# Performance work log

Hardware: AMD Instinct MI355X
Metric: run time of the kernel (lower is better)

## Reference

```python
import jax, jax.numpy as jnp
import numpy as np

N, D, DPE, H = 4096, 256, 16, 8
HD = D // H
SCALE = HD ** -0.5


def setup_inputs() -> dict:
    key = jax.random.key(0)
    ks = jax.random.split(key, 10)
    s = lambda fan_in: 1.0 / np.sqrt(fan_in)
    return {
        "x": jax.random.normal(ks[0], (N, D), jnp.float32),
        "pe": jax.random.normal(ks[1], (N, DPE), jnp.float32),
        "Wqkv": jax.random.uniform(ks[2], (D, 3 * D), jnp.float32, -s(D), s(D)),
        "bqkv": jax.random.uniform(ks[3], (3 * D,), jnp.float32, -s(D), s(D)),
        "Wpe": jax.random.uniform(ks[4], (DPE, H), jnp.float32, -s(DPE), s(DPE)),
        "bpe": jax.random.uniform(ks[5], (H,), jnp.float32, -s(DPE), s(DPE)),
        "Wout": jax.random.uniform(ks[6], (D, D), jnp.float32, -s(D), s(D)),
        "bout": jax.random.uniform(ks[7], (D,), jnp.float32, -s(D), s(D)),
    }


def reference(x, pe, Wqkv, bqkv, Wpe, bpe, Wout, bout):
    # qkv: [N, 3, H, HD] -> q,k,v each [H, N, HD]
    qkv = (x @ Wqkv + bqkv).reshape(N, 3, H, HD).transpose(1, 2, 0, 3)
    q, k, v = qkv[0], qkv[1], qkv[2]
    # attention scores [H, N, N]
    attn = jnp.einsum("hnd,hmd->hnm", q, k) * SCALE
    # pairwise PE-difference bias: bias[h,i,j] = pe_proj[i,h] - pe_proj[j,h]
    pe_proj = pe @ Wpe + bpe  # [N, H]
    pe_bias = (pe_proj[:, None, :] - pe_proj[None, :, :]).transpose(2, 0, 1)
    attn = jax.nn.softmax(attn + pe_bias, axis=-1)
    # dropout disabled (eval mode, p=0)
    out = jnp.einsum("hnm,hmd->nhd", attn, v).reshape(N, D)
    return out @ Wout + bout
```

## Files before the change

kernel.cpp:

```cpp
#include <hip/hip_runtime.h>
#include <math.h>

#define NN 4096
#define HH 8
constexpr float SCALE = 0.17677669529663687f;
constexpr float LOG2E = 1.4426950408889634f;
constexpr float SC2   = SCALE * LOG2E;

typedef __bf16 bf16;
typedef __bf16 bf16x8 __attribute__((ext_vector_type(8)));
typedef __bf16 bf16x4 __attribute__((ext_vector_type(4)));
typedef float  f32x4  __attribute__((ext_vector_type(4)));

#define MFMA(a, b, c) __builtin_amdgcn_mfma_f32_16x16x32_bf16((a), (b), (c), 0, 0, 0)

template <int K, int N, bool SCALEQ>
__device__ __forceinline__ void wcast_body(const float* __restrict__ W,
                                           bf16* __restrict__ WhT,
                                           bf16* __restrict__ WlT,
                                           int n0, int k0, int t,
                                           float (*tile)[65]) {
#pragma unroll
    for (int p = 0; p < 16; ++p) {
        const int r = p * 4 + (t >> 6);
        const int c = t & 63;
        tile[r][c] = W[(size_t)(k0 + r) * N + n0 + c];
    }
    __syncthreads();
    const int nr = t >> 2, kc0 = (t & 3) * 16;
    const float sc = (SCALEQ && (n0 + nr) < 256) ? SC2 : 1.0f;
    bf16x8 h[2], l[2];
#pragma unroll
    for (int g = 0; g < 2; ++g)
#pragma unroll
        for (int j = 0; j < 8; ++j) {
            const float v = tile[kc0 + g * 8 + j][nr] * sc;
            const bf16 hh = (bf16)v;
            h[g][j] = hh;
            l[g][j] = (bf16)(v - (float)hh);
        }
    const size_t ob = (size_t)(n0 + nr) * K + k0 + kc0;
    *(bf16x8*)&WhT[ob] = h[0];
    *(bf16x8*)&WhT[ob + 8] = h[1];
    *(bf16x8*)&WlT[ob] = l[0];
    *(bf16x8*)&WlT[ob + 8] = l[1];
}

__global__ __launch_bounds__(256) void preproc_kernel(
    const float* __restrict__ x, const float* __restrict__ Wqkv,
    const float* __restrict__ Wout, const float* __restrict__ bqkv,
    const float* __restrict__ pe, const float* __restrict__ Wpe,
    const float* __restrict__ bpe,
    bf16* __restrict__ xh, bf16* __restrict__ xl,
    bf16* __restrict__ WqkvhT, bf16* __restrict__ WqkvlT,
    bf16* __restrict__ WouthT, bf16* __restrict__ WoutlT,
    float* __restrict__ bqkv_s, float* __restrict__ ep) {
    __shared__ float tile[64][65];
    const int b = blockIdx.x, t = threadIdx.x;
    if (b < 1024) {
        const int i = (b * 256 + t) * 4;
        const float4 v = *(const float4*)&x[i];
        bf16x4 h, l;
        const float vv[4] = {v.x, v.y, v.z, v.w};
#pragma unroll
        for (int r = 0; r < 4; ++r) {
            h[r] = (bf16)vv[r];
            l[r] = (bf16)(vv[r] - (float)h[r]);
        }
        *(bf16x4*)&xh[i] = h;
        *(bf16x4*)&xl[i] = l;
    } else if (b < 1072) {
        const int bb = b - 1024;
        wcast_body<256, 768, true>(Wqkv, WqkvhT, WqkvlT, (bb % 12) * 64, (bb / 12) * 64, t, tile);
    } else if (b < 1088) {
        const int bb = b - 1072;
        wcast_body<256, 256, false>(Wout, WouthT, WoutlT, (bb % 4) * 64, (bb / 4) * 64, t, tile);
    } else if (b < 1216) {
        const int idx = (b - 1088) * 256 + t;
        const int h = idx >> 12;
        const int n = idx & 4095;
        float acc = bpe[h];
#pragma unroll
        for (int k = 0; k < 16; ++k) acc += pe[n * 16 + k] * Wpe[k * 8 + h];
        ep[h * NN + n] = __builtin_amdgcn_exp2f(-acc * LOG2E - 8.0f);
    } else {
        for (int i = t; i < 768; i += 256)
            bqkv_s[i] = bqkv[i] * (i < 256 ? SC2 : 1.0f);
    }
}

template <int NOUT, int NTILE, typename OT>
__global__ __launch_bounds__(256, 2) void gemm3s_kernel(const bf16* __restrict__ Ah,
                                                        const bf16* __restrict__ Al,
                                                        const bf16* __restrict__ BhT,
                                                        const bf16* __restrict__ BlT,
                                                        const float* __restrict__ bias,
                                                        OT* __restrict__ C) {
    constexpr int NS = NTILE / 16;
    const int t = threadIdx.x, wave = t >> 6, lane = t & 63;
    const int quad = lane >> 4, i16 = lane & 15;
    const int m0 = blockIdx.x * 128 + wave * 32;
    const int n0 = blockIdx.y * NTILE;

    __shared__ __align__(16) bf16 Bs[NTILE * 512];

    {
        const int l = t & 63, i16l = l & 15, ql = l >> 4;
#pragma unroll
        for (int c = t >> 6; c < NS * 16; c += 4) {
            const bool lo = c >= NS * 8;
            const int cc = lo ? c - NS * 8 : c;
            const int nsi = cc >> 3, kc = cc & 7;
            const bf16* src = (lo ? BlT : BhT) +
                (size_t)(n0 + nsi * 16 + i16l) * 256 + kc * 32 + ql * 8;
            *(uint4*)&Bs[c * 512 + l * 8] = *(const uint4*)src;
        }
    }

    bf16x8 ah[2][8], al[2][8];
#pragma unroll
    for (int ms = 0; ms < 2; ++ms) {
        const size_t abase = (size_t)(m0 + ms * 16 + i16) * 256 + quad * 8;
#pragma unroll
        for (int kc = 0; kc < 8; ++kc) {
            ah[ms][kc] = *(const bf16x8*)&Ah[abase + kc * 32];
            al[ms][kc] = *(const bf16x8*)&Al[abase + kc * 32];
        }
    }
    __syncthreads();

#pragma unroll
    for (int nsi = 0; nsi < NS; ++nsi) {
        f32x4 acc[2];
        acc[0] = f32x4{0.f, 0.f, 0.f, 0.f};
        acc[1] = f32x4{0.f, 0.f, 0.f, 0.f};
#pragma unroll
        for (int kc = 0; kc < 8; ++kc) {
            const bf16x8 bh = *(const bf16x8*)&Bs[(nsi * 8 + kc) * 512 + lane * 8];
            const bf16x8 bl = *(const bf16x8*)&Bs[((NS + nsi) * 8 + kc) * 512 + lane * 8];
            acc[0] = MFMA(ah[0][kc], bh, acc[0]);
            acc[0] = MFMA(ah[0][kc], bl, acc[0]);
            acc[0] = MFMA(al[0][kc], bh, acc[0]);
            acc[1] = MFMA(ah[1][kc], bh, acc[1]);
            acc[1] = MFMA(ah[1][kc], bl, acc[1]);
            acc[1] = MFMA(al[1][kc], bh, acc[1]);
        }
        const int n = n0 + nsi * 16 + i16;
        const float b = bias[n];
#pragma unroll
        for (int ms = 0; ms < 2; ++ms)
#pragma unroll
            for (int r = 0; r < 4; ++r)
                C[(size_t)(m0 + ms * 16 + quad * 4 + r) * NOUT + n] = (OT)(acc[ms][r] + b);
    }
}

__global__ __launch_bounds__(256) void kvtrans_kernel(const bf16* __restrict__ qkvb,
                                                      const float* __restrict__ ep,
                                                      bf16* __restrict__ Kf,
                                                      bf16* __restrict__ Vf) {
    const int t = threadIdx.x;
    const int kt = blockIdx.y, h = blockIdx.x;
    __shared__ __align__(16) bf16 Ktile[64 * 32];
    __shared__ __align__(16) bf16 Vtile[64 * 32];
    __shared__ float eps[64];
    {
        const int tok = kt * 64 + (t >> 2);
        const int d8 = (t & 3) * 8;
        *(uint4*)&Ktile[(t >> 2) * 32 + d8] =
            *(const uint4*)&qkvb[(size_t)tok * 768 + 256 + h * 32 + d8];
        *(uint4*)&Vtile[(t >> 2) * 32 + d8] =
            *(const uint4*)&qkvb[(size_t)tok * 768 + 512 + h * 32 + d8];
        if (t < 64) eps[t] = ep[h * NN + kt * 64 + t];
    }
    __syncthreads();
    {
        const int s = t >> 6, l = t & 63, quad = l >> 4, i16 = l & 15;
        bf16x8 o;
#pragma unroll
        for (int j = 0; j < 8; ++j) o[j] = Ktile[(s * 16 + i16) * 32 + quad * 8 + j];
        *(bf16x8*)&Kf[((size_t)(h * 64 + kt) * 4 + s) * 512 + l * 8] = o;
    }
    for (int c = t; c < 384; c += 256) {
        const int ch = c >> 6, ll = c & 63, qd = ll >> 4, ii = ll & 15;
        const int dt = ch >> 1, kc = ch & 1;
        const int dimp = dt * 16 + ii;
        bf16x8 o;
#pragma unroll
        for (int j = 0; j < 8; ++j) {
            const int key = kc * 32 + qd * 8 + j;
            float v;
            if (dimp < 32)       v = (float)Vtile[key * 32 + dimp] * eps[key];
            else if (dimp == 32) v = eps[key];
            else                 v = 0.f;
            o[j] = (bf16)v;
        }
        *(bf16x8*)&Vf[((size_t)(h * 64 + kt) * 6 + ch) * 512 + ll * 8] = o;
    }
}

__global__ __launch_bounds__(256, 2) void attn_kernel(const bf16* __restrict__ qkvb,
                                                      const bf16* __restrict__ Kf,
                                                      const bf16* __restrict__ Vf,
                                                      bf16* __restrict__ aoh,
                                                      bf16* __restrict__ aol) {
    const int t = threadIdx.x, kh = t >> 6, lane = t & 63;
    const int quad = lane >> 4, i16 = lane & 15;
    const int qb = blockIdx.y, h = blockIdx.x;

    __shared__ __align__(16) bf16 Pt[4][4][16 * 72];
    __shared__ __align__(16) float Mrg[3][64][48];

    const int q0 = qb * 64;
    bf16x8 qf[4];
#pragma unroll
    for (int qs = 0; qs < 4; ++qs)
        qf[qs] = *(const bf16x8*)&qkvb[(size_t)(q0 + qs * 16 + i16) * 768 + h * 32 + quad * 8];

    f32x4 o[3][4];
#pragma unroll
    for (int dt = 0; dt < 3; ++dt)
#pragma unroll
        for (int qs = 0; qs < 4; ++qs) o[dt][qs] = f32x4{0.f, 0.f, 0.f, 0.f};

    const bf16* kb = Kf + (size_t)(h * 64) * 2048 + lane * 8;
    const bf16* vb = Vf + (size_t)(h * 64) * 3072 + lane * 8;

    const int kt0 = kh * 16;
    bf16x8 kcur[4];
#pragma unroll
    for (int s = 0; s < 4; ++s)
        kcur[s] = *(const bf16x8*)&kb[((size_t)kt0 * 4 + s) * 512];

    for (int it = 0; it < 16; ++it) {
        const int kt = kt0 + it;
        bf16x8 vv[6];
#pragma unroll
        for (int c = 0; c < 6; ++c)
            vv[c] = *(const bf16x8*)&vb[((size_t)kt * 6 + c) * 512];
        bf16x8 knx[4];
        if (it < 15) {
#pragma unroll
            for (int s = 0; s < 4; ++s)
                knx[s] = *(const bf16x8*)&kb[((size_t)(kt + 1) * 4 + s) * 512];
        } else {
#pragma unroll
            for (int s = 0; s < 4; ++s) knx[s] = kcur[s];
        }

        const f32x4 z = {0.f, 0.f, 0.f, 0.f};
#pragma unroll
        for (int qh = 0; qh < 2; ++qh) {
            f32x4 sf[2][4];
#pragma unroll
            for (int ks = 0; ks < 4; ++ks) {
                sf[0][ks] = MFMA(kcur[ks], qf[qh * 2 + 0], z);
                sf[1][ks] = MFMA(kcur[ks], qf[qh * 2 + 1], z);
            }
#pragma unroll
            for (int qi = 0; qi < 2; ++qi) {
                const int qs = qh * 2 + qi;
#pragma unroll
                for (int ks = 0; ks < 4; ++ks) {
                    bf16x4 pk;
#pragma unroll
                    for (int r = 0; r < 4; ++r)
                        pk[r] = (bf16)__builtin_amdgcn_exp2f(sf[qi][ks][r]);
                    *(bf16x4*)&Pt[kh][qs][i16 * 72 + ks * 16 + quad * 4] = pk;
                }
            }
        }
        asm volatile("s_waitcnt lgkmcnt(0)" ::: "memory");

#pragma unroll
        for (int qs = 0; qs < 4; ++qs) {
            const bf16x8 pb0 = *(const bf16x8*)&Pt[kh][qs][i16 * 72 + 0 * 32 + quad * 8];
            const bf16x8 pb1 = *(const bf16x8*)&Pt[kh][qs][i16 * 72 + 1 * 32 + quad * 8];
#pragma unroll
            for (int dt = 0; dt < 3; ++dt) {
                o[dt][qs] = MFMA(vv[dt * 2 + 0], pb0, o[dt][qs]);
                o[dt][qs] = MFMA(vv[dt * 2 + 1], pb1, o[dt][qs]);
            }
        }
#pragma unroll
        for (int s = 0; s < 4; ++s) kcur[s] = knx[s];
    }

    if (kh != 0) {
#pragma unroll
        for (int dt = 0; dt < 3; ++dt)
#pragma unroll
            for (int qs = 0; qs < 4; ++qs)
                *(f32x4*)&Mrg[kh - 1][lane][(dt * 4 + qs) * 4] = o[dt][qs];
    }
    __syncthreads();
    if (kh == 0) {
#pragma unroll
        for (int w = 0; w < 3; ++w)
#pragma unroll
            for (int dt = 0; dt < 3; ++dt)
#pragma unroll
                for (int qs = 0; qs < 4; ++qs)
                    o[dt][qs] += *(const f32x4*)&Mrg[w][lane][(dt * 4 + qs) * 4];
#pragma unroll
        for (int qs = 0; qs < 4; ++qs) {
            const float linv = 1.0f / __shfl(o[2][qs][0], i16, 64);
            const int row = q0 + qs * 16 + i16;
#pragma unroll
            for (int dt = 0; dt < 2; ++dt) {
                bf16x4 hi, lo;
#pragma unroll
                for (int r = 0; r < 4; ++r) {
                    const float v = o[dt][qs][r] * linv;
                    hi[r] = (bf16)v;
                    lo[r] = (bf16)(v - (float)hi[r]);
                }
                const size_t ob = (size_t)row * 256 + h * 32 + dt * 16 + quad * 4;
                *(bf16x4*)&aoh[ob] = hi;
                *(bf16x4*)&aol[ob] = lo;
            }
        }
    }
}

extern "C" void kernel_launch(void* const* d_in, const int* in_sizes, int n_in,
                              void* d_out, int out_size, void* d_ws, size_t ws_size,
                              hipStream_t stream) {
    const float* x    = (const float*)d_in[0];
    const float* pe   = (const float*)d_in[1];
    const float* Wqkv = (const float*)d_in[2];
    const float* bqkv = (const float*)d_in[3];
    const float* Wpe  = (const float*)d_in[4];
    const float* bpe  = (const float*)d_in[5];
    const float* Wout = (const float*)d_in[6];
    const float* bout = (const float*)d_in[7];
    float* out = (float*)d_out;

    char* ws = (char*)d_ws;
    bf16*  xh      = (bf16*)(ws);
    bf16*  xl      = (bf16*)(ws + 2097152);
    bf16*  WqkvhT  = (bf16*)(ws + 4194304);
    bf16*  WqkvlT  = (bf16*)(ws + 4587520);
    bf16*  WouthT  = (bf16*)(ws + 4980736);
    bf16*  WoutlT  = (bf16*)(ws + 5111808);
    float* bqkv_s  = (float*)(ws + 5242880);
    bf16*  qkvb    = (bf16*)(ws + 5245952);
    float* ep      = (float*)(ws + 11537408);
    bf16*  Kf      = (bf16*)(ws + 11668480);
    bf16*  Vf      = (bf16*)(ws + 13765632);
    bf16*  aoh     = (bf16*)(ws + 16911360);
    bf16*  aol     = (bf16*)(ws + 19008512);

    preproc_kernel<<<1217, 256, 0, stream>>>(x, Wqkv, Wout, bqkv, pe, Wpe, bpe,
                                             xh, xl, WqkvhT, WqkvlT, WouthT, WoutlT,
                                             bqkv_s, ep);
    gemm3s_kernel<768, 48, bf16><<<dim3(32, 16), 256, 0, stream>>>(xh, xl, WqkvhT, WqkvlT, bqkv_s, qkvb);
    kvtrans_kernel<<<dim3(HH, 64), 256, 0, stream>>>(qkvb, ep, Kf, Vf);
    attn_kernel<<<dim3(HH, NN / 64), 256, 0, stream>>>(qkvb, Kf, Vf, aoh, aol);
    gemm3s_kernel<256, 16, float><<<dim3(32, 16), 256, 0, stream>>>(aoh, aol, WouthT, WoutlT, bout, out);
}
```

Measured before the change: 130.3 us.

## Split attention keys across blocks with atomic merge and MFMA-accumulated PE bias

The per-key PE bias no longer multiplies V as exp(bias). It is loaded as the MFMA accumulator init, so exp2 includes it directly, and the extra V column that carried the row sum is dropped. The row-sum is now accumulated in registers. The key range is split across two blocks per query tile (grid z=2), merged with fp32 atomicAdd into a zeroed buffer. Normalization and the hi/lo bf16 split move into a new output-projection GEMM that reads the fp32 partials. This cuts one third of the PV MFMAs and raises occupancy, at the cost of atomics, a zeroing pass in preproc and fp32 intermediate traffic.

```diff
diff --git a/kernel.cpp b/kernel.cpp
--- a/kernel.cpp
+++ b/kernel.cpp
@@ -54,7 +54,8 @@
     bf16* __restrict__ xh, bf16* __restrict__ xl,
     bf16* __restrict__ WqkvhT, bf16* __restrict__ WqkvlT,
     bf16* __restrict__ WouthT, bf16* __restrict__ WoutlT,
-    float* __restrict__ bqkv_s, float* __restrict__ ep) {
+    float* __restrict__ bqkv_s, float* __restrict__ ppb,
+    uint4* __restrict__ zbase) {
     __shared__ float tile[64][65];
     const int b = blockIdx.x, t = threadIdx.x;
     if (b < 1024) {
@@ -82,10 +83,12 @@
         float acc = bpe[h];
 #pragma unroll
         for (int k = 0; k < 16; ++k) acc += pe[n * 16 + k] * Wpe[k * 8 + h];
-        ep[h * NN + n] = __builtin_amdgcn_exp2f(-acc * LOG2E - 8.0f);
-    } else {
+        ppb[h * NN + n] = -acc * LOG2E - 8.0f;
+    } else if (b == 1216) {
         for (int i = t; i < 768; i += 256)
             bqkv_s[i] = bqkv[i] * (i < 256 ? SC2 : 1.0f);
+    } else {
+        zbase[(size_t)(b - 1217) * 256 + t] = uint4{0, 0, 0, 0};
     }
 }
 
@@ -156,14 +159,12 @@
 }
 
 __global__ __launch_bounds__(256) void kvtrans_kernel(const bf16* __restrict__ qkvb,
-                                                      const float* __restrict__ ep,
                                                       bf16* __restrict__ Kf,
                                                       bf16* __restrict__ Vf) {
     const int t = threadIdx.x;
     const int kt = blockIdx.y, h = blockIdx.x;
     __shared__ __align__(16) bf16 Ktile[64 * 32];
     __shared__ __align__(16) bf16 Vtile[64 * 32];
-    __shared__ float eps[64];
     {
         const int tok = kt * 64 + (t >> 2);
         const int d8 = (t & 3) * 8;
@@ -171,45 +172,36 @@
             *(const uint4*)&qkvb[(size_t)tok * 768 + 256 + h * 32 + d8];
         *(uint4*)&Vtile[(t >> 2) * 32 + d8] =
             *(const uint4*)&qkvb[(size_t)tok * 768 + 512 + h * 32 + d8];
-        if (t < 64) eps[t] = ep[h * NN + kt * 64 + t];
     }
     __syncthreads();
-    {
-        const int s = t >> 6, l = t & 63, quad = l >> 4, i16 = l & 15;
+    const int ch = t >> 6, l = t & 63, quad = l >> 4, i16 = l & 15;
+    {
         bf16x8 o;
 #pragma unroll
-        for (int j = 0; j < 8; ++j) o[j] = Ktile[(s * 16 + i16) * 32 + quad * 8 + j];
-        *(bf16x8*)&Kf[((size_t)(h * 64 + kt) * 4 + s) * 512 + l * 8] = o;
-    }
-    for (int c = t; c < 384; c += 256) {
-        const int ch = c >> 6, ll = c & 63, qd = ll >> 4, ii = ll & 15;
+        for (int j = 0; j < 8; ++j) o[j] = Ktile[(ch * 16 + i16) * 32 + quad * 8 + j];
+        *(bf16x8*)&Kf[((size_t)(h * 64 + kt) * 4 + ch) * 512 + l * 8] = o;
+    }
+    {
         const int dt = ch >> 1, kc = ch & 1;
-        const int dimp = dt * 16 + ii;
         bf16x8 o;
 #pragma unroll
-        for (int j = 0; j < 8; ++j) {
-            const int key = kc * 32 + qd * 8 + j;
-            float v;
-            if (dimp < 32)       v = (float)Vtile[key * 32 + dimp] * eps[key];
-            else if (dimp == 32) v = eps[key];
-            else                 v = 0.f;
-            o[j] = (bf16)v;
-        }
-        *(bf16x8*)&Vf[((size_t)(h * 64 + kt) * 6 + ch) * 512 + ll * 8] = o;
-    }
-}
-
-__global__ __launch_bounds__(256, 2) void attn_kernel(const bf16* __restrict__ qkvb,
+        for (int j = 0; j < 8; ++j)
+            o[j] = Vtile[(kc * 32 + quad * 8 + j) * 32 + dt * 16 + i16];
+        *(bf16x8*)&Vf[((size_t)(h * 64 + kt) * 4 + ch) * 512 + l * 8] = o;
+    }
+}
+
+__global__ __launch_bounds__(256, 3) void attn_kernel(const bf16* __restrict__ qkvb,
                                                       const bf16* __restrict__ Kf,
                                                       const bf16* __restrict__ Vf,
-                                                      bf16* __restrict__ aoh,
-                                                      bf16* __restrict__ aol) {
-    const int t = threadIdx.x, kh = t >> 6, lane = t & 63;
+                                                      const float* __restrict__ ppb,
+                                                      float* __restrict__ aof,
+                                                      float* __restrict__ lvec) {
+    const int t = threadIdx.x, w = t >> 6, lane = t & 63;
     const int quad = lane >> 4, i16 = lane & 15;
-    const int qb = blockIdx.y, h = blockIdx.x;
+    const int qb = blockIdx.y, h = blockIdx.x, ksh = blockIdx.z;
 
     __shared__ __align__(16) bf16 Pt[4][4][16 * 72];
-    __shared__ __align__(16) float Mrg[3][64][48];
 
     const int q0 = qb * 64;
     bf16x8 qf[4];
@@ -217,110 +209,160 @@
     for (int qs = 0; qs < 4; ++qs)
         qf[qs] = *(const bf16x8*)&qkvb[(size_t)(q0 + qs * 16 + i16) * 768 + h * 32 + quad * 8];
 
-    f32x4 o[3][4];
-#pragma unroll
-    for (int dt = 0; dt < 3; ++dt)
+    f32x4 o[2][4];
+#pragma unroll
+    for (int dt = 0; dt < 2; ++dt)
 #pragma unroll
         for (int qs = 0; qs < 4; ++qs) o[dt][qs] = f32x4{0.f, 0.f, 0.f, 0.f};
+    float lacc[4] = {0.f, 0.f, 0.f, 0.f};
 
     const bf16* kb = Kf + (size_t)(h * 64) * 2048 + lane * 8;
-    const bf16* vb = Vf + (size_t)(h * 64) * 3072 + lane * 8;
-
-    const int kt0 = kh * 16;
-    bf16x8 kcur[4];
-#pragma unroll
-    for (int s = 0; s < 4; ++s)
-        kcur[s] = *(const bf16x8*)&kb[((size_t)kt0 * 4 + s) * 512];
-
-    for (int it = 0; it < 16; ++it) {
+    const bf16* vb = Vf + (size_t)(h * 64) * 2048 + lane * 8;
+    const float* pph = ppb + h * NN + quad * 4;
+
+    const int kt0 = ksh * 32 + w * 8;
+    for (int it = 0; it < 8; ++it) {
         const int kt = kt0 + it;
-        bf16x8 vv[6];
-#pragma unroll
-        for (int c = 0; c < 6; ++c)
-            vv[c] = *(const bf16x8*)&vb[((size_t)kt * 6 + c) * 512];
-        bf16x8 knx[4];
-        if (it < 15) {
-#pragma unroll
-            for (int s = 0; s < 4; ++s)
-                knx[s] = *(const bf16x8*)&kb[((size_t)(kt + 1) * 4 + s) * 512];
-        } else {
-#pragma unroll
-            for (int s = 0; s < 4; ++s) knx[s] = kcur[s];
-        }
-
-        const f32x4 z = {0.f, 0.f, 0.f, 0.f};
-#pragma unroll
-        for (int qh = 0; qh < 2; ++qh) {
-            f32x4 sf[2][4];
+        bf16x8 kc4[4], vv[4];
+        f32x4 bias[4];
+#pragma unroll
+        for (int s = 0; s < 4; ++s) {
+            kc4[s] = *(const bf16x8*)&kb[((size_t)kt * 4 + s) * 512];
+            vv[s]  = *(const bf16x8*)&vb[((size_t)kt * 4 + s) * 512];
+            bias[s] = *(const f32x4*)&pph[kt * 64 + s * 16];
+        }
+
+#pragma unroll
+        for (int qs = 0; qs < 4; ++qs) {
+            f32x4 sf[4];
+#pragma unroll
+            for (int ks = 0; ks < 4; ++ks) sf[ks] = MFMA(kc4[ks], qf[qs], bias[ks]);
+            float lq = 0.f;
 #pragma unroll
             for (int ks = 0; ks < 4; ++ks) {
-                sf[0][ks] = MFMA(kcur[ks], qf[qh * 2 + 0], z);
-                sf[1][ks] = MFMA(kcur[ks], qf[qh * 2 + 1], z);
+                float p[4];
+#pragma unroll
+                for (int r = 0; r < 4; ++r) p[r] = __builtin_amdgcn_exp2f(sf[ks][r]);
+                bf16x4 pk;
+#pragma unroll
+                for (int r = 0; r < 4; ++r) pk[r] = (bf16)p[r];
+                *(bf16x4*)&Pt[w][qs][i16 * 72 + ks * 16 + quad * 4] = pk;
+                lq += (p[0] + p[1]) + (p[2] + p[3]);
             }
-#pragma unroll
-            for (int qi = 0; qi < 2; ++qi) {
-                const int qs = qh * 2 + qi;
-#pragma unroll
-                for (int ks = 0; ks < 4; ++ks) {
-                    bf16x4 pk;
-#pragma unroll
-                    for (int r = 0; r < 4; ++r)
-                        pk[r] = (bf16)__builtin_amdgcn_exp2f(sf[qi][ks][r]);
-                    *(bf16x4*)&Pt[kh][qs][i16 * 72 + ks * 16 + quad * 4] = pk;
-                }
+            lacc[qs] += lq;
+        }
+        asm volatile("s_waitcnt lgkmcnt(0)" ::: "memory");
+
+#pragma unroll
+        for (int qs = 0; qs < 4; ++qs) {
+            const bf16x8 pb0 = *(const bf16x8*)&Pt[w][qs][i16 * 72 + 0 * 32 + quad * 8];
+            const bf16x8 pb1 = *(const bf16x8*)&Pt[w][qs][i16 * 72 + 1 * 32 + quad * 8];
+            o[0][qs] = MFMA(vv[0], pb0, o[0][qs]);
+            o[0][qs] = MFMA(vv[1], pb1, o[0][qs]);
+            o[1][qs] = MFMA(vv[2], pb0, o[1][qs]);
+            o[1][qs] = MFMA(vv[3], pb1, o[1][qs]);
+        }
+    }
+
+    {
+        float* myo = (float*)&Pt[w][0][0];
+#pragma unroll
+        for (int qs = 0; qs < 4; ++qs) {
+            *(f32x4*)&myo[(qs * 64 + lane) * 8 + 0] = o[0][qs];
+            *(f32x4*)&myo[(qs * 64 + lane) * 8 + 4] = o[1][qs];
+        }
+        *(f32x4*)&myo[2048 + lane * 4] = f32x4{lacc[0], lacc[1], lacc[2], lacc[3]};
+    }
+    __syncthreads();
+    {
+        f32x4 a0 = {0.f, 0.f, 0.f, 0.f}, a1 = {0.f, 0.f, 0.f, 0.f};
+        float lw = 0.f;
+#pragma unroll
+        for (int ww = 0; ww < 4; ++ww) {
+            const float* p = (const float*)&Pt[ww][0][0];
+            a0 += *(const f32x4*)&p[(w * 64 + lane) * 8 + 0];
+            a1 += *(const f32x4*)&p[(w * 64 + lane) * 8 + 4];
+            lw += p[2048 + lane * 4 + w];
+        }
+        lw += __shfl_xor(lw, 16, 64);
+        lw += __shfl_xor(lw, 32, 64);
+        float* dst = aof + (size_t)(q0 + w * 16 + i16) * 256 + h * 32;
+#pragma unroll
+        for (int r = 0; r < 4; ++r) {
+            atomicAdd(&dst[quad * 4 + r], a0[r]);
+            atomicAdd(&dst[16 + quad * 4 + r], a1[r]);
+        }
+        if (quad == 0) atomicAdd(&lvec[h * NN + q0 + w * 16 + i16], lw);
+    }
+}
+
+__global__ __launch_bounds__(256, 2) void gemm3f_kernel(const float* __restrict__ aof,
+                                                        const float* __restrict__ lvec,
+                                                        const bf16* __restrict__ BhT,
+                                                        const bf16* __restrict__ BlT,
+                                                        const float* __restrict__ bias,
+                                                        float* __restrict__ C) {
+    const int t = threadIdx.x, wave = t >> 6, lane = t & 63;
+    const int quad = lane >> 4, i16 = lane & 15;
+    const int m0 = blockIdx.x * 128 + wave * 32;
+    const int n0 = blockIdx.y * 16;
+
+    __shared__ __align__(16) bf16 Bs[16 * 512];
+    {
+        const int l = t & 63, i16l = l & 15, ql = l >> 4;
+#pragma unroll
+        for (int c = t >> 6; c < 16; c += 4) {
+            const bool lo = c >= 8;
+            const int kc = lo ? c - 8 : c;
+            const bf16* src = (lo ? BlT : BhT) +
+                (size_t)(n0 + i16l) * 256 + kc * 32 + ql * 8;
+            *(uint4*)&Bs[c * 512 + l * 8] = *(const uint4*)src;
+        }
+    }
+
+    bf16x8 ah[2][8], al[2][8];
+#pragma unroll
+    for (int ms = 0; ms < 2; ++ms) {
+        const int row = m0 + ms * 16 + i16;
+#pragma unroll
+        for (int kc = 0; kc < 8; ++kc) {
+            const float linv = 1.0f / lvec[kc * NN + row];
+            const f32x4 u0 = *(const f32x4*)&aof[(size_t)row * 256 + kc * 32 + quad * 8];
+            const f32x4 u1 = *(const f32x4*)&aof[(size_t)row * 256 + kc * 32 + quad * 8 + 4];
+#pragma unroll
+            for (int e = 0; e < 4; ++e) {
+                const float v0 = u0[e] * linv, v1 = u1[e] * linv;
+                const bf16 h0 = (bf16)v0, h1 = (bf16)v1;
+                ah[ms][kc][e] = h0;
+                ah[ms][kc][e + 4] = h1;
+                al[ms][kc][e] = (bf16)(v0 - (float)h0);
+                al[ms][kc][e + 4] = (bf16)(v1 - (float)h1);
             }
         }
-        asm volatile("s_waitcnt lgkmcnt(0)" ::: "memory");
-
-#pragma unroll
-        for (int qs = 0; qs < 4; ++qs) {
-            const bf16x8 pb0 = *(const bf16x8*)&Pt[kh][qs][i16 * 72 + 0 * 32 + quad * 8];
-            const bf16x8 pb1 = *(const bf16x8*)&Pt[kh][qs][i16 * 72 + 1 * 32 + quad * 8];
-#pragma unroll
-            for (int dt = 0; dt < 3; ++dt) {
-                o[dt][qs] = MFMA(vv[dt * 2 + 0], pb0, o[dt][qs]);
-                o[dt][qs] = MFMA(vv[dt * 2 + 1], pb1, o[dt][qs]);
-            }
-        }
-#pragma unroll
-        for (int s = 0; s < 4; ++s) kcur[s] = knx[s];
-    }
-
-    if (kh != 0) {
-#pragma unroll
-        for (int dt = 0; dt < 3; ++dt)
-#pragma unroll
-            for (int qs = 0; qs < 4; ++qs)
-                *(f32x4*)&Mrg[kh - 1][lane][(dt * 4 + qs) * 4] = o[dt][qs];
     }
     __syncthreads();
-    if (kh == 0) {
-#pragma unroll
-        for (int w = 0; w < 3; ++w)
-#pragma unroll
-            for (int dt = 0; dt < 3; ++dt)
-#pragma unroll
-                for (int qs = 0; qs < 4; ++qs)
-                    o[dt][qs] += *(const f32x4*)&Mrg[w][lane][(dt * 4 + qs) * 4];
-#pragma unroll
-        for (int qs = 0; qs < 4; ++qs) {
-            const float linv = 1.0f / __shfl(o[2][qs][0], i16, 64);
-            const int row = q0 + qs * 16 + i16;
-#pragma unroll
-            for (int dt = 0; dt < 2; ++dt) {
-                bf16x4 hi, lo;
-#pragma unroll
-                for (int r = 0; r < 4; ++r) {
-                    const float v = o[dt][qs][r] * linv;
-                    hi[r] = (bf16)v;
-                    lo[r] = (bf16)(v - (float)hi[r]);
-                }
-                const size_t ob = (size_t)row * 256 + h * 32 + dt * 16 + quad * 4;
-                *(bf16x4*)&aoh[ob] = hi;
-                *(bf16x4*)&aol[ob] = lo;
-            }
-        }
-    }
+
+    f32x4 acc[2];
+    acc[0] = f32x4{0.f, 0.f, 0.f, 0.f};
+    acc[1] = f32x4{0.f, 0.f, 0.f, 0.f};
+#pragma unroll
+    for (int kc = 0; kc < 8; ++kc) {
+        const bf16x8 bh = *(const bf16x8*)&Bs[kc * 512 + lane * 8];
+        const bf16x8 bl = *(const bf16x8*)&Bs[(8 + kc) * 512 + lane * 8];
+        acc[0] = MFMA(ah[0][kc], bh, acc[0]);
+        acc[0] = MFMA(ah[0][kc], bl, acc[0]);
+        acc[0] = MFMA(al[0][kc], bh, acc[0]);
+        acc[1] = MFMA(ah[1][kc], bh, acc[1]);
+        acc[1] = MFMA(ah[1][kc], bl, acc[1]);
+        acc[1] = MFMA(al[1][kc], bh, acc[1]);
+    }
+    const int n = n0 + i16;
+    const float b = bias[n];
+#pragma unroll
+    for (int ms = 0; ms < 2; ++ms)
+#pragma unroll
+        for (int r = 0; r < 4; ++r)
+            C[(size_t)(m0 + ms * 16 + quad * 4 + r) * 256 + n] = acc[ms][r] + b;
 }
 
 extern "C" void kernel_launch(void* const* d_in, const int* in_sizes, int n_in,
@@ -345,17 +387,18 @@
     bf16*  WoutlT  = (bf16*)(ws + 5111808);
     float* bqkv_s  = (float*)(ws + 5242880);
     bf16*  qkvb    = (bf16*)(ws + 5245952);
-    float* ep      = (float*)(ws + 11537408);
+    float* ppb     = (float*)(ws + 11537408);
     bf16*  Kf      = (bf16*)(ws + 11668480);
     bf16*  Vf      = (bf16*)(ws + 13765632);
-    bf16*  aoh     = (bf16*)(ws + 16911360);
-    bf16*  aol     = (bf16*)(ws + 19008512);
-
-    preproc_kernel<<<1217, 256, 0, stream>>>(x, Wqkv, Wout, bqkv, pe, Wpe, bpe,
+    float* aof     = (float*)(ws + 15862784);
+    float* lvec    = (float*)(ws + 20057088);
+    uint4* zbase   = (uint4*)(ws + 15862784);
+
+    preproc_kernel<<<2273, 256, 0, stream>>>(x, Wqkv, Wout, bqkv, pe, Wpe, bpe,
                                              xh, xl, WqkvhT, WqkvlT, WouthT, WoutlT,
-                                             bqkv_s, ep);
+                                             bqkv_s, ppb, zbase);
     gemm3s_kernel<768, 48, bf16><<<dim3(32, 16), 256, 0, stream>>>(xh, xl, WqkvhT, WqkvlT, bqkv_s, qkvb);
-    kvtrans_kernel<<<dim3(HH, 64), 256, 0, stream>>>(qkvb, ep, Kf, Vf);
-    attn_kernel<<<dim3(HH, NN / 64), 256, 0, stream>>>(qkvb, Kf, Vf, aoh, aol);
-    gemm3s_kernel<256, 16, float><<<dim3(32, 16), 256, 0, stream>>>(aoh, aol, WouthT, WoutlT, bout, out);
-}
+    kvtrans_kernel<<<dim3(HH, 64), 256, 0, stream>>>(qkvb, Kf, Vf);
+    attn_kernel<<<dim3(HH, NN / 64, 2), 256, 0, stream>>>(qkvb, Kf, Vf, ppb, aof, lvec);
+    gemm3f_kernel<<<dim3(32, 16), 256, 0, stream>>>(aof, lvec, WouthT, WoutlT, bout, out);
+}
```

After: 153.8 us. 1.18x slower.

## Split attention keys across two blocks and merge partials in output GEMM

Applied to the files above, without the earlier changes.

The attention grid gains a z-dimension of two, so each block covers half of the keys, with four waves doing 8 key tiles each instead of 16. Each block reduces its waves' partials through the P shared buffer and writes unnormalized fp32 partial outputs and row sums to workspace. A new output-projection GEMM sums the two partials, normalizes, splits into bf16 hi/lo and runs the 3-pass MFMA. This doubles the attention parallelism and raises launch bounds to 3 blocks per CU, at the cost of extra fp32 global traffic for the partials.

```diff
diff --git a/kernel.cpp b/kernel.cpp
--- a/kernel.cpp
+++ b/kernel.cpp
@@ -199,17 +199,18 @@
     }
 }
 
-__global__ __launch_bounds__(256, 2) void attn_kernel(const bf16* __restrict__ qkvb,
+__global__ __launch_bounds__(256, 3) void attn_kernel(const bf16* __restrict__ qkvb,
                                                       const bf16* __restrict__ Kf,
                                                       const bf16* __restrict__ Vf,
-                                                      bf16* __restrict__ aoh,
-                                                      bf16* __restrict__ aol) {
-    const int t = threadIdx.x, kh = t >> 6, lane = t & 63;
+                                                      float* __restrict__ aof0,
+                                                      float* __restrict__ aof1,
+                                                      float* __restrict__ lv0,
+                                                      float* __restrict__ lv1) {
+    const int t = threadIdx.x, w = t >> 6, lane = t & 63;
     const int quad = lane >> 4, i16 = lane & 15;
-    const int qb = blockIdx.y, h = blockIdx.x;
+    const int qb = blockIdx.y, h = blockIdx.x, ksh = blockIdx.z;
 
     __shared__ __align__(16) bf16 Pt[4][4][16 * 72];
-    __shared__ __align__(16) float Mrg[3][64][48];
 
     const int q0 = qb * 64;
     bf16x8 qf[4];
@@ -226,20 +227,20 @@
     const bf16* kb = Kf + (size_t)(h * 64) * 2048 + lane * 8;
     const bf16* vb = Vf + (size_t)(h * 64) * 3072 + lane * 8;
 
-    const int kt0 = kh * 16;
+    const int kt0 = ksh * 32 + w * 8;
     bf16x8 kcur[4];
 #pragma unroll
     for (int s = 0; s < 4; ++s)
         kcur[s] = *(const bf16x8*)&kb[((size_t)kt0 * 4 + s) * 512];
 
-    for (int it = 0; it < 16; ++it) {
+    for (int it = 0; it < 8; ++it) {
         const int kt = kt0 + it;
         bf16x8 vv[6];
 #pragma unroll
         for (int c = 0; c < 6; ++c)
             vv[c] = *(const bf16x8*)&vb[((size_t)kt * 6 + c) * 512];
         bf16x8 knx[4];
-        if (it < 15) {
+        if (it < 7) {
 #pragma unroll
             for (int s = 0; s < 4; ++s)
                 knx[s] = *(const bf16x8*)&kb[((size_t)(kt + 1) * 4 + s) * 512];
@@ -266,7 +267,7 @@
 #pragma unroll
                     for (int r = 0; r < 4; ++r)
                         pk[r] = (bf16)__builtin_amdgcn_exp2f(sf[qi][ks][r]);
-                    *(bf16x4*)&Pt[kh][qs][i16 * 72 + ks * 16 + quad * 4] = pk;
+                    *(bf16x4*)&Pt[w][qs][i16 * 72 + ks * 16 + quad * 4] = pk;
                 }
             }
         }
@@ -274,8 +275,8 @@
 
 #pragma unroll
         for (int qs = 0; qs < 4; ++qs) {
-            const bf16x8 pb0 = *(const bf16x8*)&Pt[kh][qs][i16 * 72 + 0 * 32 + quad * 8];
-            const bf16x8 pb1 = *(const bf16x8*)&Pt[kh][qs][i16 * 72 + 1 * 32 + quad * 8];
+            const bf16x8 pb0 = *(const bf16x8*)&Pt[w][qs][i16 * 72 + 0 * 32 + quad * 8];
+            const bf16x8 pb1 = *(const bf16x8*)&Pt[w][qs][i16 * 72 + 1 * 32 + quad * 8];
 #pragma unroll
             for (int dt = 0; dt < 3; ++dt) {
                 o[dt][qs] = MFMA(vv[dt * 2 + 0], pb0, o[dt][qs]);
@@ -286,41 +287,108 @@
         for (int s = 0; s < 4; ++s) kcur[s] = knx[s];
     }
 
-    if (kh != 0) {
-#pragma unroll
-        for (int dt = 0; dt < 3; ++dt)
+    {
+        float* myo = (float*)&Pt[w][0][0];
+#pragma unroll
+        for (int qs = 0; qs < 4; ++qs) {
+            *(f32x4*)&myo[(qs * 64 + lane) * 8 + 0] = o[0][qs];
+            *(f32x4*)&myo[(qs * 64 + lane) * 8 + 4] = o[1][qs];
+        }
+        if (quad == 0) {
 #pragma unroll
             for (int qs = 0; qs < 4; ++qs)
-                *(f32x4*)&Mrg[kh - 1][lane][(dt * 4 + qs) * 4] = o[dt][qs];
+                myo[2048 + qs * 16 + i16] = o[2][qs][0];
+        }
     }
     __syncthreads();
-    if (kh == 0) {
-#pragma unroll
-        for (int w = 0; w < 3; ++w)
-#pragma unroll
-            for (int dt = 0; dt < 3; ++dt)
-#pragma unroll
-                for (int qs = 0; qs < 4; ++qs)
-                    o[dt][qs] += *(const f32x4*)&Mrg[w][lane][(dt * 4 + qs) * 4];
-#pragma unroll
-        for (int qs = 0; qs < 4; ++qs) {
-            const float linv = 1.0f / __shfl(o[2][qs][0], i16, 64);
-            const int row = q0 + qs * 16 + i16;
-#pragma unroll
-            for (int dt = 0; dt < 2; ++dt) {
-                bf16x4 hi, lo;
-#pragma unroll
-                for (int r = 0; r < 4; ++r) {
-                    const float v = o[dt][qs][r] * linv;
-                    hi[r] = (bf16)v;
-                    lo[r] = (bf16)(v - (float)hi[r]);
-                }
-                const size_t ob = (size_t)row * 256 + h * 32 + dt * 16 + quad * 4;
-                *(bf16x4*)&aoh[ob] = hi;
-                *(bf16x4*)&aol[ob] = lo;
+    {
+        f32x4 a0 = {0.f, 0.f, 0.f, 0.f}, a1 = {0.f, 0.f, 0.f, 0.f};
+        float lsum = 0.f;
+#pragma unroll
+        for (int ww = 0; ww < 4; ++ww) {
+            const float* p = (const float*)&Pt[ww][0][0];
+            a0 += *(const f32x4*)&p[(w * 64 + lane) * 8 + 0];
+            a1 += *(const f32x4*)&p[(w * 64 + lane) * 8 + 4];
+            if (lane < 16) lsum += p[2048 + w * 16 + lane];
+        }
+        float* aof = ksh ? aof1 : aof0;
+        float* dst = aof + (size_t)(q0 + w * 16 + i16) * 256 + h * 32;
+        *(f32x4*)&dst[quad * 4] = a0;
+        *(f32x4*)&dst[16 + quad * 4] = a1;
+        if (lane < 16) (ksh ? lv1 : lv0)[h * NN + q0 + w * 16 + lane] = lsum;
+    }
+}
+
+__global__ __launch_bounds__(256, 2) void gemm3f_kernel(const float* __restrict__ aof0,
+                                                        const float* __restrict__ aof1,
+                                                        const float* __restrict__ lv0,
+                                                        const float* __restrict__ lv1,
+                                                        const bf16* __restrict__ BhT,
+                                                        const bf16* __restrict__ BlT,
+                                                        const float* __restrict__ bias,
+                                                        float* __restrict__ C) {
+    const int t = threadIdx.x, wave = t >> 6, lane = t & 63;
+    const int quad = lane >> 4, i16 = lane & 15;
+    const int m0 = blockIdx.x * 128 + wave * 32;
+    const int n0 = blockIdx.y * 16;
+
+    __shared__ __align__(16) bf16 Bs[16 * 512];
+    {
+        const int l = t & 63, i16l = l & 15, ql = l >> 4;
+#pragma unroll
+        for (int c = t >> 6; c < 16; c += 4) {
+            const bool lo = c >= 8;
+            const int kc = lo ? c - 8 : c;
+            const bf16* src = (lo ? BlT : BhT) +
+                (size_t)(n0 + i16l) * 256 + kc * 32 + ql * 8;
+            *(uint4*)&Bs[c * 512 + l * 8] = *(const uint4*)src;
+        }
+    }
+
+    bf16x8 ah[2][8], al[2][8];
+#pragma unroll
+    for (int ms = 0; ms < 2; ++ms) {
+        const int row = m0 + ms * 16 + i16;
+#pragma unroll
+        for (int kc = 0; kc < 8; ++kc) {
+            const float linv = 1.0f / (lv0[kc * NN + row] + lv1[kc * NN + row]);
+            const size_t ab = (size_t)row * 256 + kc * 32 + quad * 8;
+            const f32x4 u0 = *(const f32x4*)&aof0[ab] + *(const f32x4*)&aof1[ab];
+            const f32x4 u1 = *(const f32x4*)&aof0[ab + 4] + *(const f32x4*)&aof1[ab + 4];
+#pragma unroll
+            for (int e = 0; e < 4; ++e) {
+                const float v0 = u0[e] * linv, v1 = u1[e] * linv;
+                const bf16 h0 = (bf16)v0, h1 = (bf16)v1;
+                ah[ms][kc][e] = h0;
+                ah[ms][kc][e + 4] = h1;
+                al[ms][kc][e] = (bf16)(v0 - (float)h0);
+                al[ms][kc][e + 4] = (bf16)(v1 - (float)h1);
             }
         }
     }
+    __syncthreads();
+
+    f32x4 acc[2];
+    acc[0] = f32x4{0.f, 0.f, 0.f, 0.f};
+    acc[1] = f32x4{0.f, 0.f, 0.f, 0.f};
+#pragma unroll
+    for (int kc = 0; kc < 8; ++kc) {
+        const bf16x8 bh = *(const bf16x8*)&Bs[kc * 512 + lane * 8];
+        const bf16x8 bl = *(const bf16x8*)&Bs[(8 + kc) * 512 + lane * 8];
+        acc[0] = MFMA(ah[0][kc], bh, acc[0]);
+        acc[0] = MFMA(ah[0][kc], bl, acc[0]);
+        acc[0] = MFMA(al[0][kc], bh, acc[0]);
+        acc[1] = MFMA(ah[1][kc], bh, acc[1]);
+        acc[1] = MFMA(ah[1][kc], bl, acc[1]);
+        acc[1] = MFMA(al[1][kc], bh, acc[1]);
+    }
+    const int n = n0 + i16;
+    const float b = bias[n];
+#pragma unroll
+    for (int ms = 0; ms < 2; ++ms)
+#pragma unroll
+        for (int r = 0; r < 4; ++r)
+            C[(size_t)(m0 + ms * 16 + quad * 4 + r) * 256 + n] = acc[ms][r] + b;
 }
 
 extern "C" void kernel_launch(void* const* d_in, const int* in_sizes, int n_in,
@@ -348,14 +416,16 @@
     float* ep      = (float*)(ws + 11537408);
     bf16*  Kf      = (bf16*)(ws + 11668480);
     bf16*  Vf      = (bf16*)(ws + 13765632);
-    bf16*  aoh     = (bf16*)(ws + 16911360);
-    bf16*  aol     = (bf16*)(ws + 19008512);
+    float* aof0    = (float*)(ws + 16911360);
+    float* aof1    = (float*)(ws + 21105664);
+    float* lv0     = (float*)(ws + 25299968);
+    float* lv1     = (float*)(ws + 25431040);
 
     preproc_kernel<<<1217, 256, 0, stream>>>(x, Wqkv, Wout, bqkv, pe, Wpe, bpe,
                                              xh, xl, WqkvhT, WqkvlT, WouthT, WoutlT,
                                              bqkv_s, ep);
     gemm3s_kernel<768, 48, bf16><<<dim3(32, 16), 256, 0, stream>>>(xh, xl, WqkvhT, WqkvlT, bqkv_s, qkvb);
     kvtrans_kernel<<<dim3(HH, 64), 256, 0, stream>>>(qkvb, ep, Kf, Vf);
-    attn_kernel<<<dim3(HH, NN / 64), 256, 0, stream>>>(qkvb, Kf, Vf, aoh, aol);
-    gemm3s_kernel<256, 16, float><<<dim3(32, 16), 256, 0, stream>>>(aoh, aol, WouthT, WoutlT, bout, out);
-}
+    attn_kernel<<<dim3(HH, NN / 64, 2), 256, 0, stream>>>(qkvb, Kf, Vf, aof0, aof1, lv0, lv1);
+    gemm3f_kernel<<<dim3(32, 16), 256, 0, stream>>>(aof0, aof1, lv0, lv1, WouthT, WoutlT, bout, out);
+}
```

Result: slower. 150.6 us (+15.6%).
